# Kernel tuning notes

Measured on AMD Instinct MI355X. Metric: run time of the kernel, lower is better.

Reference implementation:

```python
import jax, jax.numpy as jnp
import numpy as np

TOP_K = 2


def setup_inputs() -> dict:
    key = jax.random.key(0)
    k1, k2, k3, k4 = jax.random.split(key, 4)
    B, D, H, E = 16384, 1024, 1024, 8
    return {
        "x": jax.random.normal(k1, (B, D), dtype=jnp.float32),
        "Wv": jax.random.normal(k2, (E, D, H), dtype=jnp.float32),
        "Wg": jax.random.normal(k3, (E, D, H), dtype=jnp.float32),
        "gate_w": jax.random.normal(k4, (E, D), dtype=jnp.float32) * (1.0 / np.sqrt(D)),
        "gate_b": jnp.zeros((E,), dtype=jnp.float32),
    }


def reference(x, Wv, Wg, gate_w, gate_b):
    # Router: softmax over expert logits, then top-k selection.
    logits = x @ gate_w.T + gate_b                      # [B, E]
    probs = jax.nn.softmax(logits, axis=1)
    topk_scores, topk_idx = jax.lax.top_k(probs, TOP_K)  # [B, K]

    B, E = probs.shape
    # Scatter top-k scores into a dense [B, E] combine matrix (zeros elsewhere).
    combine = jnp.zeros((B, E), dtype=probs.dtype).at[
        jnp.arange(B)[:, None], topk_idx
    ].add(topk_scores)

    # Dense per-expert SwiGLU; combine matrix zeros out non-selected experts,
    # so the math matches the grouped-gemm top-k dispatch exactly.
    v = jnp.einsum("bd,edh->beh", x, Wv)                # [B, E, H]
    g = jnp.einsum("bd,edh->beh", x, Wg)                # [B, E, H]
    act = v * jax.nn.sigmoid(g)                         # SwiGLU-style gating
    return jnp.einsum("be,beh->bh", combine, act)       # weighted combine [B, H]
```

## Files before the change

kernel.cpp:

```cpp
#include <hip/hip_runtime.h>

#define D_DIM 1024
#define H_DIM 1024
#define E_NUM 8
#define BM 256
#define BN 256
#define BK 64
#define NT (D_DIM / BK)
#define CAP 5120
#define RT_TOK 32

typedef __attribute__((ext_vector_type(8))) _Float16 h8v;
typedef __attribute__((ext_vector_type(4))) float f4v;

__device__ __forceinline__ unsigned short f2h(float f) {
  union { _Float16 h; unsigned short u; } c;
  c.h = (_Float16)f;
  return c.u;
}

__device__ __forceinline__ void gl2lds16(const void* g, void* l) {
  __builtin_amdgcn_global_load_lds(
      (const __attribute__((address_space(1))) unsigned int*)g,
      (__attribute__((address_space(3))) unsigned int*)l, 16, 0, 0);
}

__device__ __forceinline__ unsigned ldsaddr(const void* p) {
  return (unsigned)(unsigned long long)(const __attribute__((address_space(3))) void*)p;
}

__global__ __launch_bounds__(256) void transpose_w_kernel(
    const float* __restrict__ Wv, const float* __restrict__ Wg,
    unsigned short* __restrict__ Wc) {
  __shared__ float tile[64][65];
  int z = blockIdx.z;
  const float* W = (z & 1) ? Wg : Wv;
  int mat = z & 1;
  int e = z >> 1;
  int h0 = blockIdx.x * 64, d0 = blockIdx.y * 64;
  const float* Wp = W + (size_t)e * D_DIM * H_DIM;
  unsigned short* Wcp = Wc + (size_t)e * (2 * H_DIM) * D_DIM;
  int t = threadIdx.x;
#pragma unroll
  for (int j = 0; j < 4; j++) {
    int id = t + 256 * j;
    int dd = id >> 4, hc = id & 15;
    float4 v = *(const float4*)(Wp + (size_t)(d0 + dd) * H_DIM + h0 + hc * 4);
    tile[dd][hc * 4 + 0] = v.x;
    tile[dd][hc * 4 + 1] = v.y;
    tile[dd][hc * 4 + 2] = v.z;
    tile[dd][hc * 4 + 3] = v.w;
  }
  __syncthreads();
#pragma unroll
  for (int j = 0; j < 2; j++) {
    int id = t + 256 * j;
    int h_ = id >> 3, dc = id & 7;
    unsigned short tmp[8];
#pragma unroll
    for (int k = 0; k < 8; k++) tmp[k] = f2h(tile[dc * 8 + k][h_]);
    int hg = h0 + h_;
    int ng = ((hg >> 4) << 5) | (mat << 4) | (hg & 15);
    *(uint4*)(Wcp + (size_t)ng * D_DIM + d0 + dc * 8) = *(uint4*)tmp;
  }
}

__global__ __launch_bounds__(256) void router_kernel(
    const float4* __restrict__ x4, const float4* __restrict__ gw4,
    const float* __restrict__ gb, int* __restrict__ counts,
    int* __restrict__ bucket, float* __restrict__ scoreB,
    int* __restrict__ slotOf, ushort4* __restrict__ xh4, int B) {
  __shared__ float4 gwS[E_NUM * 256];
  __shared__ short eSelS[RT_TOK][2];
  __shared__ float sSelS[RT_TOK][2];
  __shared__ int lCnt[E_NUM], lBase[E_NUM];
  __shared__ unsigned char lOff[RT_TOK][2];
  int tid = threadIdx.x;
  for (int i = tid; i < E_NUM * 256; i += 256) gwS[i] = gw4[i];
  if (tid < E_NUM) lCnt[tid] = 0;
  __syncthreads();
  int wid = tid >> 6, lane = tid & 63;
  for (int rep = 0; rep < RT_TOK / 4; rep++) {
    int t = wid * (RT_TOK / 4) + rep;
    int b = blockIdx.x * RT_TOK + t;
    float acc[E_NUM];
#pragma unroll
    for (int e = 0; e < E_NUM; e++) acc[e] = 0.0f;
#pragma unroll
    for (int i = 0; i < 4; i++) {
      float4 xv = x4[(size_t)b * 256 + i * 64 + lane];
      ushort4 o;
      o.x = f2h(xv.x); o.y = f2h(xv.y); o.z = f2h(xv.z); o.w = f2h(xv.w);
      xh4[(size_t)b * 256 + i * 64 + lane] = o;
#pragma unroll
      for (int e = 0; e < E_NUM; e++) {
        float4 w = gwS[e * 256 + i * 64 + lane];
        acc[e] += xv.x * w.x + xv.y * w.y + xv.z * w.z + xv.w * w.w;
      }
    }
#pragma unroll
    for (int e = 0; e < E_NUM; e++) {
#pragma unroll
      for (int off = 32; off > 0; off >>= 1) acc[e] += __shfl_down(acc[e], off);
    }
    if (lane == 0) {
      float l[E_NUM];
#pragma unroll
      for (int e = 0; e < E_NUM; e++) l[e] = acc[e] + gb[e];
      int i0 = 0;
#pragma unroll
      for (int e = 1; e < E_NUM; e++) if (l[e] > l[i0]) i0 = e;
      int i1 = (i0 == 0) ? 1 : 0;
#pragma unroll
      for (int e = 0; e < E_NUM; e++) if (e != i0 && l[e] > l[i1]) i1 = e;
      float mx = l[i0];
      float denom = 0.0f;
#pragma unroll
      for (int e = 0; e < E_NUM; e++) denom += __expf(l[e] - mx);
      eSelS[t][0] = (short)i0; sSelS[t][0] = 1.0f / denom;
      eSelS[t][1] = (short)i1; sSelS[t][1] = __expf(l[i1] - mx) / denom;
    }
  }
  __syncthreads();
  if (tid < RT_TOK) {
    lOff[tid][0] = (unsigned char)atomicAdd(&lCnt[eSelS[tid][0]], 1);
    lOff[tid][1] = (unsigned char)atomicAdd(&lCnt[eSelS[tid][1]], 1);
  }
  __syncthreads();
  if (tid < E_NUM) lBase[tid] = atomicAdd(&counts[tid * 32], lCnt[tid]);
  __syncthreads();
  if (tid < RT_TOK) {
    int b = blockIdx.x * RT_TOK + tid;
#pragma unroll
    for (int j = 0; j < 2; j++) {
      int e = eSelS[tid][j];
      int pos = lBase[e] + lOff[tid][j];
      if (pos < CAP) {
        int slot = e * CAP + pos;
        bucket[slot] = b;
        scoreB[slot] = sSelS[tid][j];
        slotOf[b * 2 + j] = slot;
      }
    }
  }
}


#define DSR(dst, areg, IMM)                                                   \
  asm volatile("ds_read_b128 %0, %1 offset:%c2"                               \
               : "=v"(dst) : "v"(areg), "i"(IMM))

#define OFFS(CB, HI) ((CB) * 32768 + (HI) * 16384)

#define RD12_P0(CB) do {                                                      \
    DSR(bf[0][0], bB0, OFFS(CB, 0) + 0);                                      \
    DSR(bf[1][0], bB0, OFFS(CB, 0) + 2048);                                   \
    DSR(af[0][0], aA0, OFFS(CB, 0) + 0);                                      \
    DSR(af[1][0], aA0, OFFS(CB, 0) + 2048);                                   \
    DSR(af[2][0], aA0, OFFS(CB, 0) + 4096);                                   \
    DSR(af[3][0], aA0, OFFS(CB, 0) + 6144);                                   \
    DSR(bf[0][1], bB1, OFFS(CB, 0) + 0);                                      \
    DSR(bf[1][1], bB1, OFFS(CB, 0) + 2048);                                   \
    DSR(af[0][1], aA1, OFFS(CB, 0) + 0);                                      \
    DSR(af[1][1], aA1, OFFS(CB, 0) + 2048);                                   \
    DSR(af[2][1], aA1, OFFS(CB, 0) + 4096);                                   \
    DSR(af[3][1], aA1, OFFS(CB, 0) + 6144);                                   \
  } while (0)

#define RD8_A(CB, HI) do {                                                    \
    DSR(af[0][0], aA0, OFFS(CB, HI) + 0);                                     \
    DSR(af[1][0], aA0, OFFS(CB, HI) + 2048);                                  \
    DSR(af[2][0], aA0, OFFS(CB, HI) + 4096);                                  \
    DSR(af[3][0], aA0, OFFS(CB, HI) + 6144);                                  \
    DSR(af[0][1], aA1, OFFS(CB, HI) + 0);                                     \
    DSR(af[1][1], aA1, OFFS(CB, HI) + 2048);                                  \
    DSR(af[2][1], aA1, OFFS(CB, HI) + 4096);                                  \
    DSR(af[3][1], aA1, OFFS(CB, HI) + 6144);                                  \
  } while (0)

#define RD4_B(CB, HI) do {                                                    \
    DSR(bf[0][0], bB0, OFFS(CB, HI) + 0);                                     \
    DSR(bf[1][0], bB0, OFFS(CB, HI) + 2048);                                  \
    DSR(bf[0][1], bB1, OFFS(CB, HI) + 0);                                     \
    DSR(bf[1][1], bB1, OFFS(CB, HI) + 2048);                                  \
  } while (0)

#define MFMA_S(MO, NO, S)                                                     \
  {                                                                           \
    _Pragma("unroll") for (int m = 0; m < 4; m++) {                           \
      _Pragma("unroll") for (int n = 0; n < 2; n++) {                         \
        acc[(MO) + m][(NO) + n] = __builtin_amdgcn_mfma_f32_16x16x32_f16(     \
            af[m][S], bf[n][S], acc[(MO) + m][(NO) + n], 0, 0, 0);            \
      }                                                                       \
    }                                                                         \
  }

#define PH_BAR() __builtin_amdgcn_s_barrier()
#define LGKM(N) do {                                                          \
    asm volatile("s_waitcnt lgkmcnt(" #N ")" ::: "memory");                   \
    __builtin_amdgcn_sched_barrier(0);                                        \
  } while (0)
#define VMW(N) asm volatile("s_waitcnt vmcnt(" #N ")" ::: "memory")
#define PRIO1() __builtin_amdgcn_s_setprio(1)
#define PRIO0() __builtin_amdgcn_s_setprio(0)

#define TILE_N(CB) do {                                                       \
                           \
    RD12_P0(CB);                                                              \
    gl2lds16(pA[0], &As[(CB) ^ 1][0 * 4096 + dst0]);                          \
    gl2lds16(pA[1], &As[(CB) ^ 1][1 * 4096 + dst0]);                          \
    LGKM(6);  PRIO1(); MFMA_S(0, 0, 0); PRIO0();                              \
    LGKM(0);  PRIO1(); MFMA_S(0, 0, 1); PRIO0();                              \
    VMW(4); PH_BAR();                                                         \
                               \
    RD4_B(CB, 1);                                                             \
    gl2lds16(pB[0], &Bs[(CB) ^ 1][0 * 4096 + dst0]);                          \
    gl2lds16(pB[1], &Bs[(CB) ^ 1][1 * 4096 + dst0]);                          \
    LGKM(2);  PRIO1(); MFMA_S(0, 2, 0); PRIO0();                              \
    LGKM(0);  PRIO1(); MFMA_S(0, 2, 1); PRIO0();                              \
    VMW(4); PH_BAR();                                                         \
                   \
    RD8_A(CB, 1);                                                             \
    gl2lds16(pB[2], &Bs[(CB) ^ 1][2 * 4096 + dst0]);                          \
    gl2lds16(pB[3], &Bs[(CB) ^ 1][3 * 4096 + dst0]);                          \
    LGKM(4);  PRIO1(); MFMA_S(4, 2, 0); PRIO0();                              \
    LGKM(0);  PRIO1(); MFMA_S(4, 2, 1); PRIO0();                              \
                     \
    RD4_B(CB, 0);                                                             \
    gl2lds16(pA[2], &As[(CB) ^ 1][2 * 4096 + dst0]);                          \
    gl2lds16(pA[3], &As[(CB) ^ 1][3 * 4096 + dst0]);                          \
    LGKM(2);  PRIO1(); MFMA_S(4, 0, 0); PRIO0();                              \
    LGKM(0);  PRIO1(); MFMA_S(4, 0, 1); PRIO0();                              \
    VMW(4); PH_BAR();                                                         \
    _Pragma("unroll") for (int i = 0; i < 4; i++) { pA[i] += BK; pB[i] += BK; } \
  } while (0)

template <bool USE_PARTIAL>
__global__ __launch_bounds__(512, 2) void moe_gemm_kernel(
    const unsigned short* __restrict__ xh, const unsigned short* __restrict__ Wc,
    const int* __restrict__ counts, const int* __restrict__ bucket,
    const float* __restrict__ scoreB, _Float16* __restrict__ partial,
    float* __restrict__ out, int B) {
  int o = blockIdx.x + 20 * (blockIdx.y + 8 * blockIdx.z);
  int e = o & 7;
  int r = o >> 3;
  int m0 = (r % 20) * BM;
  int nt_ = r / 20;
  int n0 = nt_ * BN;
  int cnt = counts[e * 32];
  if (m0 >= cnt) return;

  __shared__ unsigned short As[2][BM * BK];
  __shared__ unsigned short Bs[2][BN * BK];
  __shared__ int tokS[BM];
  __shared__ float scS[BM];

  int tid = threadIdx.x;
  if (tid < BM) {
    int gr = m0 + tid;
    bool vld = gr < cnt;
    tokS[tid] = vld ? bucket[e * CAP + gr] : 0;
    scS[tid] = vld ? scoreB[e * CAP + gr] : 0.0f;
  }
  __syncthreads();

  int wid = tid >> 6, lane = tid & 63;
  int wm = wid & 1, wn = wid >> 1;
  int quad = lane >> 4, lr = lane & 15;

  int rA = tid >> 3;
  int ksw = ((tid & 7) ^ (rA & 7)) * 8;
  const unsigned short* WcE = Wc + (size_t)e * (2 * H_DIM) * D_DIM;
  const unsigned short* pA[4];
  const unsigned short* pB[4];
#pragma unroll
  for (int i = 0; i < 4; i++) {
    pA[i] = xh + (size_t)tokS[i * 64 + rA] * D_DIM + ksw;
    pB[i] = WcE + (size_t)(n0 + i * 64 + rA) * D_DIM + ksw;
  }
  int dst0 = tid * 8;

  unsigned swz0 = (unsigned)(((0 * 4 + quad) ^ (lr & 7)) * 16);
  unsigned swz1 = (unsigned)(((1 * 4 + quad) ^ (lr & 7)) * 16);
  unsigned ldsA = ldsaddr(&As[0][0]);
  unsigned ldsB = ldsaddr(&Bs[0][0]);
  unsigned aA0 = ldsA + (unsigned)(wm * 8192 + lr * 128) + swz0;
  unsigned aA1 = ldsA + (unsigned)(wm * 8192 + lr * 128) + swz1;
  unsigned bB0 = ldsB + (unsigned)(wn * 4096 + lr * 128) + swz0;
  unsigned bB1 = ldsB + (unsigned)(wn * 4096 + lr * 128) + swz1;

  f4v acc[8][4];
#pragma unroll
  for (int m = 0; m < 8; m++)
#pragma unroll
    for (int n = 0; n < 4; n++) acc[m][n] = (f4v){0.f, 0.f, 0.f, 0.f};

  gl2lds16(pA[0], &As[0][0 * 4096 + dst0]);
  gl2lds16(pA[1], &As[0][1 * 4096 + dst0]);
  gl2lds16(pB[0], &Bs[0][0 * 4096 + dst0]);
  gl2lds16(pB[1], &Bs[0][1 * 4096 + dst0]);
  gl2lds16(pB[2], &Bs[0][2 * 4096 + dst0]);
  gl2lds16(pB[3], &Bs[0][3 * 4096 + dst0]);
  gl2lds16(pA[2], &As[0][2 * 4096 + dst0]);
  gl2lds16(pA[3], &As[0][3 * 4096 + dst0]);
#pragma unroll
  for (int i = 0; i < 4; i++) { pA[i] += BK; pB[i] += BK; }
  VMW(4);
  PH_BAR();

  h8v af[4][2], bf[2][2];

  for (int it = 0; it < 7; ++it) {
    TILE_N(0);
    TILE_N(1);
  }
  TILE_N(0);

  {
    RD12_P0(1);
    LGKM(6);  PRIO1(); MFMA_S(0, 0, 0); PRIO0();
    LGKM(0);  PRIO1(); MFMA_S(0, 0, 1); PRIO0();
    VMW(2); PH_BAR();
    RD4_B(1, 1);
    LGKM(2);  PRIO1(); MFMA_S(0, 2, 0); PRIO0();
    LGKM(0);  PRIO1(); MFMA_S(0, 2, 1); PRIO0();
    VMW(0); PH_BAR();
    RD8_A(1, 1);
    LGKM(4);  PRIO1(); MFMA_S(4, 2, 0); PRIO0();
    LGKM(0);  PRIO1(); MFMA_S(4, 2, 1); PRIO0();
    RD4_B(1, 0);
    LGKM(2);  PRIO1(); MFMA_S(4, 0, 0); PRIO0();
    LGKM(0);  PRIO1(); MFMA_S(4, 0, 1); PRIO0();
  }

  int hb = nt_ * 128 + wn * 16 + lr;
#pragma unroll
  for (int m = 0; m < 8; m++) {
    int rb = ((m < 4) ? (wm * 64 + m * 16) : (128 + wm * 64 + (m - 4) * 16)) + quad * 4;
#pragma unroll
    for (int r2 = 0; r2 < 4; r2++) {
      int rr = rb + r2;
      float sc = scS[rr];
      if (USE_PARTIAL) {
        _Float16* pr = partial + (size_t)(e * CAP + m0 + rr) * H_DIM;
#pragma unroll
        for (int p = 0; p < 2; p++) {
          float v = acc[m][2 * p][r2];
          float g = acc[m][2 * p + 1][r2];
          pr[hb + p * 64] = (_Float16)(v * sc / (1.0f + __expf(-g)));
        }
      } else {
        int tok = tokS[rr];
#pragma unroll
        for (int p = 0; p < 2; p++) {
          float v = acc[m][2 * p][r2];
          float g = acc[m][2 * p + 1][r2];
          atomicAdd(&out[(size_t)tok * H_DIM + hb + p * 64],
                    v * sc / (1.0f + __expf(-g)));
        }
      }
    }
  }
}

__global__ __launch_bounds__(256) void gather_kernel(
    const _Float16* __restrict__ partial, const int* __restrict__ slotOf,
    float* __restrict__ out) {
  int b = blockIdx.x * 2 + (threadIdx.x >> 7);
  int t = threadIdx.x & 127;
  int s0 = slotOf[b * 2], s1 = slotOf[b * 2 + 1];
  if ((unsigned)s0 >= E_NUM * CAP) s0 = 0;
  if ((unsigned)s1 >= E_NUM * CAP) s1 = 0;
  h8v a = ((const h8v*)(partial + (size_t)s0 * H_DIM))[t];
  h8v c = ((const h8v*)(partial + (size_t)s1 * H_DIM))[t];
  float4 o0, o1;
  o0.x = (float)a[0] + (float)c[0];
  o0.y = (float)a[1] + (float)c[1];
  o0.z = (float)a[2] + (float)c[2];
  o0.w = (float)a[3] + (float)c[3];
  o1.x = (float)a[4] + (float)c[4];
  o1.y = (float)a[5] + (float)c[5];
  o1.z = (float)a[6] + (float)c[6];
  o1.w = (float)a[7] + (float)c[7];
  float4* op = (float4*)(out + (size_t)b * H_DIM);
  op[t * 2] = o0;
  op[t * 2 + 1] = o1;
}

extern "C" void kernel_launch(void* const* d_in, const int* in_sizes, int n_in,
                              void* d_out, int out_size, void* d_ws, size_t ws_size,
                              hipStream_t stream) {
  const float* x = (const float*)d_in[0];
  const float* Wv = (const float*)d_in[1];
  const float* Wg = (const float*)d_in[2];
  const float* gw = (const float*)d_in[3];
  const float* gb = (const float*)d_in[4];
  float* out = (float*)d_out;
  const int B = in_sizes[0] / D_DIM;

  char* ws = (char*)d_ws;
  unsigned short* xh = (unsigned short*)ws;
  size_t off = (size_t)B * D_DIM * 2;
  unsigned short* Wc = (unsigned short*)(ws + off);
  off += (size_t)E_NUM * (2 * H_DIM) * D_DIM * 2;
  int* counts = (int*)(ws + off);
  off += 4096;
  int* bucket = (int*)(ws + off);
  off += (size_t)E_NUM * CAP * 4;
  float* scoreB = (float*)(ws + off);
  off += (size_t)E_NUM * CAP * 4;
  int* slotOf = (int*)(ws + off);
  off += (size_t)B * 2 * 4;
  _Float16* partial = (_Float16*)(ws + off);
  size_t need = off + (size_t)E_NUM * CAP * H_DIM * 2;
  bool use_partial = ws_size >= need;

  hipMemsetAsync(counts, 0, 4096, stream);
  if (!use_partial) hipMemsetAsync(d_out, 0, (size_t)out_size * 4, stream);

  router_kernel<<<B / RT_TOK, 256, 0, stream>>>(
      (const float4*)x, (const float4*)gw, gb, counts, bucket, scoreB, slotOf,
      (ushort4*)xh, B);
  transpose_w_kernel<<<dim3(H_DIM / 64, D_DIM / 64, 2 * E_NUM), 256, 0, stream>>>(
      Wv, Wg, Wc);
  if (use_partial) {
    moe_gemm_kernel<true><<<dim3(CAP / BM, (2 * H_DIM) / BN, E_NUM), 512, 0, stream>>>(
        xh, Wc, counts, bucket, scoreB, partial, out, B);
    gather_kernel<<<B / 2, 256, 0, stream>>>(partial, slotOf, out);
  } else {
    moe_gemm_kernel<false><<<dim3(CAP / BM, (2 * H_DIM) / BN, E_NUM), 512, 0, stream>>>(
        xh, Wc, counts, bucket, scoreB, partial, out, B);
  }
}
```

Baseline: 356.6 us.

## Shrink MoE GEMM tile to 128x128 with 256 threads and a simpler pipeline

```diff
diff --git a/kernel.cpp b/kernel.cpp
--- a/kernel.cpp
+++ b/kernel.cpp
@@ -3,11 +3,13 @@
 #define D_DIM 1024
 #define H_DIM 1024
 #define E_NUM 8
-#define BM 256
-#define BN 256
+#define BM 128
+#define BN 128
 #define BK 64
 #define NT (D_DIM / BK)
 #define CAP 5120
+#define MT (CAP / BM)
+#define NTL ((2 * H_DIM) / BN)
 #define RT_TOK 32
 
 typedef __attribute__((ext_vector_type(8))) _Float16 h8v;
@@ -150,50 +152,44 @@
   asm volatile("ds_read_b128 %0, %1 offset:%c2"                               \
                : "=v"(dst) : "v"(areg), "i"(IMM))
 
-#define OFFS(CB, HI) ((CB) * 32768 + (HI) * 16384)
-
-#define RD12_P0(CB) do {                                                      \
-    DSR(bf[0][0], bB0, OFFS(CB, 0) + 0);                                      \
-    DSR(bf[1][0], bB0, OFFS(CB, 0) + 2048);                                   \
-    DSR(af[0][0], aA0, OFFS(CB, 0) + 0);                                      \
-    DSR(af[1][0], aA0, OFFS(CB, 0) + 2048);                                   \
-    DSR(af[2][0], aA0, OFFS(CB, 0) + 4096);                                   \
-    DSR(af[3][0], aA0, OFFS(CB, 0) + 6144);                                   \
-    DSR(bf[0][1], bB1, OFFS(CB, 0) + 0);                                      \
-    DSR(bf[1][1], bB1, OFFS(CB, 0) + 2048);                                   \
-    DSR(af[0][1], aA1, OFFS(CB, 0) + 0);                                      \
-    DSR(af[1][1], aA1, OFFS(CB, 0) + 2048);                                   \
-    DSR(af[2][1], aA1, OFFS(CB, 0) + 4096);                                   \
-    DSR(af[3][1], aA1, OFFS(CB, 0) + 6144);                                   \
-  } while (0)
-
-#define RD8_A(CB, HI) do {                                                    \
-    DSR(af[0][0], aA0, OFFS(CB, HI) + 0);                                     \
-    DSR(af[1][0], aA0, OFFS(CB, HI) + 2048);                                  \
-    DSR(af[2][0], aA0, OFFS(CB, HI) + 4096);                                  \
-    DSR(af[3][0], aA0, OFFS(CB, HI) + 6144);                                  \
-    DSR(af[0][1], aA1, OFFS(CB, HI) + 0);                                     \
-    DSR(af[1][1], aA1, OFFS(CB, HI) + 2048);                                  \
-    DSR(af[2][1], aA1, OFFS(CB, HI) + 4096);                                  \
-    DSR(af[3][1], aA1, OFFS(CB, HI) + 6144);                                  \
-  } while (0)
-
-#define RD4_B(CB, HI) do {                                                    \
-    DSR(bf[0][0], bB0, OFFS(CB, HI) + 0);                                     \
-    DSR(bf[1][0], bB0, OFFS(CB, HI) + 2048);                                  \
-    DSR(bf[0][1], bB1, OFFS(CB, HI) + 0);                                     \
-    DSR(bf[1][1], bB1, OFFS(CB, HI) + 2048);                                  \
-  } while (0)
-
-#define MFMA_S(MO, NO, S)                                                     \
-  {                                                                           \
+#define RD16(CB) do {                                                         \
+    DSR(af[0][0], aA0, (CB) * 16384 + 0);                                     \
+    DSR(af[1][0], aA0, (CB) * 16384 + 2048);                                  \
+    DSR(af[2][0], aA0, (CB) * 16384 + 4096);                                  \
+    DSR(af[3][0], aA0, (CB) * 16384 + 6144);                                  \
+    DSR(bf[0][0], bB0, (CB) * 16384 + 0);                                     \
+    DSR(bf[1][0], bB0, (CB) * 16384 + 2048);                                  \
+    DSR(bf[2][0], bB0, (CB) * 16384 + 4096);                                  \
+    DSR(bf[3][0], bB0, (CB) * 16384 + 6144);                                  \
+    DSR(af[0][1], aA1, (CB) * 16384 + 0);                                     \
+    DSR(af[1][1], aA1, (CB) * 16384 + 2048);                                  \
+    DSR(af[2][1], aA1, (CB) * 16384 + 4096);                                  \
+    DSR(af[3][1], aA1, (CB) * 16384 + 6144);                                  \
+    DSR(bf[0][1], bB1, (CB) * 16384 + 0);                                     \
+    DSR(bf[1][1], bB1, (CB) * 16384 + 2048);                                  \
+    DSR(bf[2][1], bB1, (CB) * 16384 + 4096);                                  \
+    DSR(bf[3][1], bB1, (CB) * 16384 + 6144);                                  \
+  } while (0)
+
+#define MFMA16(S) do {                                                        \
     _Pragma("unroll") for (int m = 0; m < 4; m++) {                           \
-      _Pragma("unroll") for (int n = 0; n < 2; n++) {                         \
-        acc[(MO) + m][(NO) + n] = __builtin_amdgcn_mfma_f32_16x16x32_f16(     \
-            af[m][S], bf[n][S], acc[(MO) + m][(NO) + n], 0, 0, 0);            \
+      _Pragma("unroll") for (int n = 0; n < 4; n++) {                         \
+        acc[m][n] = __builtin_amdgcn_mfma_f32_16x16x32_f16(                   \
+            af[m][S], bf[n][S], acc[m][n], 0, 0, 0);                          \
       }                                                                       \
     }                                                                         \
-  }
+  } while (0)
+
+#define STG8(NB) do {                                                         \
+    gl2lds16(pA[0], (char*)As + (NB) * 16384 + 0 * 4096 + dstB);              \
+    gl2lds16(pA[1], (char*)As + (NB) * 16384 + 1 * 4096 + dstB);              \
+    gl2lds16(pA[2], (char*)As + (NB) * 16384 + 2 * 4096 + dstB);              \
+    gl2lds16(pA[3], (char*)As + (NB) * 16384 + 3 * 4096 + dstB);              \
+    gl2lds16(pB[0], (char*)Bs + (NB) * 16384 + 0 * 4096 + dstB);              \
+    gl2lds16(pB[1], (char*)Bs + (NB) * 16384 + 1 * 4096 + dstB);              \
+    gl2lds16(pB[2], (char*)Bs + (NB) * 16384 + 2 * 4096 + dstB);              \
+    gl2lds16(pB[3], (char*)Bs + (NB) * 16384 + 3 * 4096 + dstB);              \
+  } while (0)
 
 #define PH_BAR() __builtin_amdgcn_s_barrier()
 #define LGKM(N) do {                                                          \
@@ -204,48 +200,29 @@
 #define PRIO1() __builtin_amdgcn_s_setprio(1)
 #define PRIO0() __builtin_amdgcn_s_setprio(0)
 
-#define TILE_N(CB) do {                                                       \
-                           \
-    RD12_P0(CB);                                                              \
-    gl2lds16(pA[0], &As[(CB) ^ 1][0 * 4096 + dst0]);                          \
-    gl2lds16(pA[1], &As[(CB) ^ 1][1 * 4096 + dst0]);                          \
-    LGKM(6);  PRIO1(); MFMA_S(0, 0, 0); PRIO0();                              \
-    LGKM(0);  PRIO1(); MFMA_S(0, 0, 1); PRIO0();                              \
-    VMW(4); PH_BAR();                                                         \
-                               \
-    RD4_B(CB, 1);                                                             \
-    gl2lds16(pB[0], &Bs[(CB) ^ 1][0 * 4096 + dst0]);                          \
-    gl2lds16(pB[1], &Bs[(CB) ^ 1][1 * 4096 + dst0]);                          \
-    LGKM(2);  PRIO1(); MFMA_S(0, 2, 0); PRIO0();                              \
-    LGKM(0);  PRIO1(); MFMA_S(0, 2, 1); PRIO0();                              \
-    VMW(4); PH_BAR();                                                         \
-                   \
-    RD8_A(CB, 1);                                                             \
-    gl2lds16(pB[2], &Bs[(CB) ^ 1][2 * 4096 + dst0]);                          \
-    gl2lds16(pB[3], &Bs[(CB) ^ 1][3 * 4096 + dst0]);                          \
-    LGKM(4);  PRIO1(); MFMA_S(4, 2, 0); PRIO0();                              \
-    LGKM(0);  PRIO1(); MFMA_S(4, 2, 1); PRIO0();                              \
-                     \
-    RD4_B(CB, 0);                                                             \
-    gl2lds16(pA[2], &As[(CB) ^ 1][2 * 4096 + dst0]);                          \
-    gl2lds16(pA[3], &As[(CB) ^ 1][3 * 4096 + dst0]);                          \
-    LGKM(2);  PRIO1(); MFMA_S(4, 0, 0); PRIO0();                              \
-    LGKM(0);  PRIO1(); MFMA_S(4, 0, 1); PRIO0();                              \
-    VMW(4); PH_BAR();                                                         \
-    _Pragma("unroll") for (int i = 0; i < 4; i++) { pA[i] += BK; pB[i] += BK; } \
+#define TILE128(CB, STG) do {                                                 \
+    RD16(CB);                                                                 \
+    if (STG) STG8((CB) ^ 1);                                                  \
+    LGKM(8); PRIO1(); MFMA16(0); PRIO0();                                     \
+    LGKM(0); PRIO1(); MFMA16(1); PRIO0();                                     \
+    if (STG) VMW(0);          \
+    PH_BAR();                                                                 \
+    if (STG) {                                                                \
+      _Pragma("unroll") for (int i = 0; i < 4; i++) { pA[i] += BK; pB[i] += BK; } \
+    }                                                                         \
   } while (0)
 
 template <bool USE_PARTIAL>
-__global__ __launch_bounds__(512, 2) void moe_gemm_kernel(
+__global__ __launch_bounds__(256, 2) void moe_gemm_kernel(
     const unsigned short* __restrict__ xh, const unsigned short* __restrict__ Wc,
     const int* __restrict__ counts, const int* __restrict__ bucket,
     const float* __restrict__ scoreB, _Float16* __restrict__ partial,
     float* __restrict__ out, int B) {
-  int o = blockIdx.x + 20 * (blockIdx.y + 8 * blockIdx.z);
+  int o = blockIdx.x;
   int e = o & 7;
   int r = o >> 3;
-  int m0 = (r % 20) * BM;
-  int nt_ = r / 20;
+  int m0 = (r % MT) * BM;
+  int nt_ = r / MT;
   int n0 = nt_ * BN;
   int cnt = counts[e * 32];
   if (m0 >= cnt) return;
@@ -275,10 +252,10 @@
   const unsigned short* pB[4];
 #pragma unroll
   for (int i = 0; i < 4; i++) {
-    pA[i] = xh + (size_t)tokS[i * 64 + rA] * D_DIM + ksw;
-    pB[i] = WcE + (size_t)(n0 + i * 64 + rA) * D_DIM + ksw;
-  }
-  int dst0 = tid * 8;
+    pA[i] = xh + (size_t)tokS[i * 32 + rA] * D_DIM + ksw;
+    pB[i] = WcE + (size_t)(n0 + i * 32 + rA) * D_DIM + ksw;
+  }
+  int dstB = tid * 16;
 
   unsigned swz0 = (unsigned)(((0 * 4 + quad) ^ (lr & 7)) * 16);
   unsigned swz1 = (unsigned)(((1 * 4 + quad) ^ (lr & 7)) * 16);
@@ -286,57 +263,34 @@
   unsigned ldsB = ldsaddr(&Bs[0][0]);
   unsigned aA0 = ldsA + (unsigned)(wm * 8192 + lr * 128) + swz0;
   unsigned aA1 = ldsA + (unsigned)(wm * 8192 + lr * 128) + swz1;
-  unsigned bB0 = ldsB + (unsigned)(wn * 4096 + lr * 128) + swz0;
-  unsigned bB1 = ldsB + (unsigned)(wn * 4096 + lr * 128) + swz1;
-
-  f4v acc[8][4];
-#pragma unroll
-  for (int m = 0; m < 8; m++)
+  unsigned bB0 = ldsB + (unsigned)(wn * 8192 + lr * 128) + swz0;
+  unsigned bB1 = ldsB + (unsigned)(wn * 8192 + lr * 128) + swz1;
+
+  f4v acc[4][4];
+#pragma unroll
+  for (int m = 0; m < 4; m++)
 #pragma unroll
     for (int n = 0; n < 4; n++) acc[m][n] = (f4v){0.f, 0.f, 0.f, 0.f};
 
-  gl2lds16(pA[0], &As[0][0 * 4096 + dst0]);
-  gl2lds16(pA[1], &As[0][1 * 4096 + dst0]);
-  gl2lds16(pB[0], &Bs[0][0 * 4096 + dst0]);
-  gl2lds16(pB[1], &Bs[0][1 * 4096 + dst0]);
-  gl2lds16(pB[2], &Bs[0][2 * 4096 + dst0]);
-  gl2lds16(pB[3], &Bs[0][3 * 4096 + dst0]);
-  gl2lds16(pA[2], &As[0][2 * 4096 + dst0]);
-  gl2lds16(pA[3], &As[0][3 * 4096 + dst0]);
+  STG8(0);
 #pragma unroll
   for (int i = 0; i < 4; i++) { pA[i] += BK; pB[i] += BK; }
-  VMW(4);
+  VMW(0);
   PH_BAR();
 
-  h8v af[4][2], bf[2][2];
+  h8v af[4][2], bf[4][2];
 
   for (int it = 0; it < 7; ++it) {
-    TILE_N(0);
-    TILE_N(1);
-  }
-  TILE_N(0);
-
-  {
-    RD12_P0(1);
-    LGKM(6);  PRIO1(); MFMA_S(0, 0, 0); PRIO0();
-    LGKM(0);  PRIO1(); MFMA_S(0, 0, 1); PRIO0();
-    VMW(2); PH_BAR();
-    RD4_B(1, 1);
-    LGKM(2);  PRIO1(); MFMA_S(0, 2, 0); PRIO0();
-    LGKM(0);  PRIO1(); MFMA_S(0, 2, 1); PRIO0();
-    VMW(0); PH_BAR();
-    RD8_A(1, 1);
-    LGKM(4);  PRIO1(); MFMA_S(4, 2, 0); PRIO0();
-    LGKM(0);  PRIO1(); MFMA_S(4, 2, 1); PRIO0();
-    RD4_B(1, 0);
-    LGKM(2);  PRIO1(); MFMA_S(4, 0, 0); PRIO0();
-    LGKM(0);  PRIO1(); MFMA_S(4, 0, 1); PRIO0();
-  }
-
-  int hb = nt_ * 128 + wn * 16 + lr;
-#pragma unroll
-  for (int m = 0; m < 8; m++) {
-    int rb = ((m < 4) ? (wm * 64 + m * 16) : (128 + wm * 64 + (m - 4) * 16)) + quad * 4;
+    TILE128(0, 1);
+    TILE128(1, 1);
+  }
+  TILE128(0, 1);
+  TILE128(1, 0);
+
+  int hb = nt_ * 64 + wn * 32 + lr;
+#pragma unroll
+  for (int m = 0; m < 4; m++) {
+    int rb = wm * 64 + m * 16 + quad * 4;
 #pragma unroll
     for (int r2 = 0; r2 < 4; r2++) {
       int rr = rb + r2;
@@ -347,7 +301,7 @@
         for (int p = 0; p < 2; p++) {
           float v = acc[m][2 * p][r2];
           float g = acc[m][2 * p + 1][r2];
-          pr[hb + p * 64] = (_Float16)(v * sc / (1.0f + __expf(-g)));
+          pr[hb + p * 16] = (_Float16)(v * sc / (1.0f + __expf(-g)));
         }
       } else {
         int tok = tokS[rr];
@@ -355,7 +309,7 @@
         for (int p = 0; p < 2; p++) {
           float v = acc[m][2 * p][r2];
           float g = acc[m][2 * p + 1][r2];
-          atomicAdd(&out[(size_t)tok * H_DIM + hb + p * 64],
+          atomicAdd(&out[(size_t)tok * H_DIM + hb + p * 16],
                     v * sc / (1.0f + __expf(-g)));
         }
       }
@@ -424,11 +378,11 @@
   transpose_w_kernel<<<dim3(H_DIM / 64, D_DIM / 64, 2 * E_NUM), 256, 0, stream>>>(
       Wv, Wg, Wc);
   if (use_partial) {
-    moe_gemm_kernel<true><<<dim3(CAP / BM, (2 * H_DIM) / BN, E_NUM), 512, 0, stream>>>(
+    moe_gemm_kernel<true><<<E_NUM * MT * NTL, 256, 0, stream>>>(
         xh, Wc, counts, bucket, scoreB, partial, out, B);
     gather_kernel<<<B / 2, 256, 0, stream>>>(partial, slotOf, out);
   } else {
-    moe_gemm_kernel<false><<<dim3(CAP / BM, (2 * H_DIM) / BN, E_NUM), 512, 0, stream>>>(
+    moe_gemm_kernel<false><<<E_NUM * MT * NTL, 256, 0, stream>>>(
         xh, Wc, counts, bucket, scoreB, partial, out, B);
   }
 }
```

Result: slower. 364.3 us (+2.2%).
